# Kernel optimization log

Measured on AMD Instinct MI355X. Metric: run time of the kernel, lower is better.

The kernel has to match this reference:

```python
import jax, jax.numpy as jnp
import numpy as np

NU, NI, E = 100000, 20000, 250000
H, HEADS, D, L = 128, 2, 64, 2


def setup_inputs() -> dict:
    key = jax.random.key(0)
    ks = jax.random.split(key, 12)
    s = 0.05  # glorot-ish init scale
    return {
        "x_user": jax.random.normal(ks[0], (NU, 64), jnp.float32),
        "x_item": jax.random.normal(ks[1], (NI, 128), jnp.float32),
        "Wp_user": jax.random.normal(ks[2], (64, H), jnp.float32) * s,
        "bp_user": jnp.zeros((H,), jnp.float32),
        "Wp_item": jax.random.normal(ks[3], (128, H), jnp.float32) * s,
        "bp_item": jnp.zeros((H,), jnp.float32),
        # stacked per [layer, relation] params; rel 0 = user->item, rel 1 = item->user
        "Wl": jax.random.normal(ks[4], (L, 2, H, H), jnp.float32) * s,  # source linear
        "bl": jnp.zeros((L, 2, H), jnp.float32),
        "Wr": jax.random.normal(ks[5], (L, 2, H, H), jnp.float32) * s,  # target linear
        "br": jnp.zeros((L, 2, H), jnp.float32),
        "att": jax.random.normal(ks[6], (L, 2, HEADS, D), jnp.float32) * s,
        "bias": jnp.zeros((L, 2, H), jnp.float32),
        "edge_src": jax.random.randint(ks[7], (E,), 0, NU, jnp.int32),  # user index per edge
        "edge_dst": jax.random.randint(ks[8], (E,), 0, NI, jnp.int32),  # item index per edge
    }


def _gatv2(x_src, x_dst, src, dst, wl, bl_, wr, br_, a, b_, n_dst):
    """One bipartite GATv2Conv (heads=HEADS, out=D, concat=True, eval mode)."""
    xl = (x_src @ wl + bl_).reshape(-1, HEADS, D)  # [Ns, h, d]
    xr = (x_dst @ wr + br_).reshape(-1, HEADS, D)  # [Nd, h, d]
    e = jax.nn.leaky_relu(xl[src] + xr[dst], 0.2)  # [E, h, d]
    logits = jnp.einsum('ehd,hd->eh', e, a)        # [E, h]
    # segment softmax over destination nodes (numerically stable)
    amax = jax.lax.stop_gradient(jax.ops.segment_max(logits, dst, num_segments=n_dst))
    p = jnp.exp(logits - amax[dst])
    denom = jax.ops.segment_sum(p, dst, num_segments=n_dst)
    alpha = p / (denom[dst] + 1e-16)               # PyG softmax epsilon
    msg = xl[src] * alpha[:, :, None]              # [E, h, d]
    out = jax.ops.segment_sum(msg, dst, num_segments=n_dst)  # [Nd, h, d]
    return out.reshape(n_dst, HEADS * D) + b_


def reference(x_user, x_item, Wp_user, bp_user, Wp_item, bp_item,
              Wl, bl, Wr, br, att, bias, edge_src, edge_dst):
    zu = x_user @ Wp_user + bp_user  # [NU, H]
    zi = x_item @ Wp_item + bp_item  # [NI, H]
    for l in range(L):
        zi_new = _gatv2(zu, zi, edge_src, edge_dst,
                        Wl[l, 0], bl[l, 0], Wr[l, 0], br[l, 0], att[l, 0], bias[l, 0], NI)
        zu_new = _gatv2(zi, zu, edge_dst, edge_src,
                        Wl[l, 1], bl[l, 1], Wr[l, 1], br[l, 1], att[l, 1], bias[l, 1], NU)
        zu, zi = zu_new, zi_new
        if l < L - 1:
            zu, zi = jax.nn.relu(zu), jax.nn.relu(zi)  # dropout is identity in eval
    return zu, zi
```

## Files before the change

kernel.cpp:

```cpp
#include <hip/hip_runtime.h>

#define HDIM 128

typedef __attribute__((ext_vector_type(8))) short short8;
typedef __attribute__((ext_vector_type(4))) float float4v;

__device__ __forceinline__ float b2f(unsigned short u){
  return __uint_as_float(((unsigned int)u) << 16);
}
__device__ __forceinline__ unsigned short f2b(float f){
  unsigned int x = __float_as_uint(f);
  x += 0x7fffu + ((x >> 16) & 1u);
  return (unsigned short)(x >> 16);
}

#if __has_builtin(__builtin_amdgcn_exp2f)
#define EXPX(x) __builtin_amdgcn_exp2f(x)
#define LOGSCALE 1.4426950408889634f
#else
#define EXPX(x) __expf(x)
#define LOGSCALE 1.f
#endif

__device__ __forceinline__ float dpp_red8(float x){
  x += __int_as_float(__builtin_amdgcn_update_dpp(0, __float_as_int(x), 0xB1, 0xF, 0xF, true));
  x += __int_as_float(__builtin_amdgcn_update_dpp(0, __float_as_int(x), 0x4E, 0xF, 0xF, true));
  x += __int_as_float(__builtin_amdgcn_update_dpp(0, __float_as_int(x), 0x141, 0xF, 0xF, true));
  return x;
}

__device__ __forceinline__ int sniff_block(const unsigned short* __restrict__ x){
  const int tid = threadIdx.x;
  int cnt = 0, tot = 0;
  for (int i = tid * 2; i < 4096; i += 512){
    float v = fabsf(b2f(x[i]));
    tot++;
    if (v > 1e-4f && v < 50.f) cnt++;
  }
  __shared__ int s_cnt[256], s_tot[256];
  s_cnt[tid] = cnt; s_tot[tid] = tot;
  __syncthreads();
  for (int o = 128; o > 0; o >>= 1){
    if (tid < o){ s_cnt[tid] += s_cnt[tid + o]; s_tot[tid] += s_tot[tid + o]; }
    __syncthreads();
  }
  __shared__ int res;
  if (tid == 0) res = (s_cnt[0] * 2 < s_tot[0]) ? 1 : 0;
  __syncthreads();
  return res;
}

#define P_WPU 0
#define P_WPI 8192
#define P_WL  24576
#define P_WR  90112
#define P_BL  155648
#define P_BR  156160
#define P_ATT 156672
#define P_BIA 157184
#define P_BPU 157696
#define P_BPI 157824
#define P_TOT 157952

struct CvtArgs { const void* src[10]; int len[10]; const unsigned short* xsniff; };

__global__ void cvt_all_kernel(CvtArgs args, unsigned short* __restrict__ P,
                               int* __restrict__ flag,
                               int* __restrict__ zero1, int nz1,
                               int* __restrict__ zero2, int nz2){
  const int f32 = sniff_block(args.xsniff);
  int t = blockIdx.x * 256 + threadIdx.x;
  if (t < nz1) zero1[t] = 0;
  if (t < nz2) zero2[t] = 0;
  if (t == 0) flag[0] = f32;
  if (t >= P_TOT) return;
  int local = t;
  int i = 0;
  while (local >= args.len[i]){ local -= args.len[i]; i++; }
  if (f32) P[t] = f2b(((const float*)args.src[i])[local]);
  else     P[t] = ((const unsigned short*)args.src[i])[local];
}

__global__ void prep_weights_kernel(const unsigned short* __restrict__ P,
                                    unsigned short* __restrict__ Wc)
{
  const int t = blockIdx.x * 256 + threadIdx.x;
  if (t >= 49664) return;
  const unsigned short* Wl = P + P_WL;
  const unsigned short* Wr = P + P_WR;
  const unsigned short* Bm[4] = { Wl, Wr + 16384, Wl + 16384, Wr };
  const unsigned short* Av[4] = { P + P_WPU, P + P_WPU, P + P_WPI, P + P_WPI };
  const unsigned short* bv[4] = { P + P_BPU, P + P_BPU, P + P_BPI, P + P_BPI };
  const unsigned short* bo[4] = { P + P_BL, P + P_BR + 128, P + P_BL + 128, P + P_BR };
  if (t < 49152){
    int job, base;
    if (t < 8192)       { job = 0; base = 0; }
    else if (t < 16384) { job = 1; base = 8192; }
    else if (t < 32768) { job = 2; base = 16384; }
    else                { job = 3; base = 32768; }
    const int local = t - base;
    const int k = local >> 7, n = local & 127;
    const unsigned short* A = Av[job] + (size_t)k * 128;
    const unsigned short* B = Bm[job];
    float s = 0.f;
    #pragma unroll 4
    for (int h = 0; h < 128; h++) s = fmaf(b2f(A[h]), b2f(B[h * 128 + n]), s);
    Wc[t] = f2b(s);
  } else {
    const int local = t - 49152;
    const int job = local >> 7, n = local & 127;
    const unsigned short* B = Bm[job];
    float s = b2f(bo[job][n]);
    for (int h = 0; h < 128; h++) s = fmaf(b2f(bv[job][h]), b2f(B[h * 128 + n]), s);
    Wc[t] = f2b(s);
  }
}

struct PermBiasArgs { const unsigned short* W0[4]; const unsigned short* W1[4];
                      int KS[4]; int base[4]; int n[4];
                      const unsigned short* blo[4]; const unsigned short* bhi[4]; };
__global__ void permute_bias_kernel(PermBiasArgs pa, unsigned short* __restrict__ dst,
                                    unsigned short* __restrict__ dstB){
  int t = blockIdx.x * 256 + threadIdx.x;
  if (t >= 114688){
    int u = t - 114688;
    if (u < 1024){
      int set = u >> 8, c = u & 255;
      dstB[u] = (c < 128) ? pa.blo[set][c] : pa.bhi[set][c - 128];
    }
    return;
  }
  int job = 0;
  while (job < 4 && t >= pa.base[job] + pa.n[job]) job++;
  if (job >= 4) return;
  int local = t - pa.base[job];
  int KS = pa.KS[job];
  int j = local & 7, rest = local >> 3;
  int l = rest & 63; rest >>= 6;
  int ks = rest % KS, tile = rest / KS;
  int k = ks * 32 + (l >> 4) * 8 + j;
  int c = tile * 16 + (l & 15);
  dst[t] = (c < 128) ? pa.W0[job][k * 128 + c] : pa.W1[job][k * 128 + (c - 128)];
}

template<int K>
__device__ __forceinline__ void linear_body(const void* __restrict__ Xv, int xstride,
                                            bool f32,
                                            const unsigned short* __restrict__ Bp,
                                            const unsigned short* __restrict__ bias,
                                            unsigned short* __restrict__ Y, int M, int bx,
                                            unsigned short* __restrict__ lds)
{
  constexpr int KS = K / 32;
  constexpr int LK = K + 8;
  constexpr int ROUNDS = (32 * K) / 2048;
  const int wave = threadIdx.x >> 6, lane = threadIdx.x & 63;
  const int quad = lane >> 4, l16 = lane & 15;
  const int row0 = bx * 32;

  #pragma unroll
  for (int rd = 0; rd < ROUNDS; rd++){
    const int e = rd * 2048 + (int)threadIdx.x * 8;
    const int rr = e / K, cc = e % K;
    int grow = row0 + rr; if (grow >= M) grow = M - 1;
    unsigned short* dst = lds + rr * LK + cc;
    if (f32){
      const float* p = (const float*)Xv + (size_t)grow * xstride + cc;
      float4 v0 = *(const float4*)p;
      float4 v1 = *(const float4*)(p + 4);
      short8 tmp;
      tmp[0] = (short)f2b(v0.x); tmp[1] = (short)f2b(v0.y);
      tmp[2] = (short)f2b(v0.z); tmp[3] = (short)f2b(v0.w);
      tmp[4] = (short)f2b(v1.x); tmp[5] = (short)f2b(v1.y);
      tmp[6] = (short)f2b(v1.z); tmp[7] = (short)f2b(v1.w);
      *(short8*)dst = tmp;
    } else {
      *(short8*)dst = *(const short8*)((const unsigned short*)Xv + (size_t)grow * xstride + cc);
    }
  }
  __syncthreads();

  float4v acc[2][4];
  const float4v z = {0.f, 0.f, 0.f, 0.f};
  #pragma unroll
  for (int i = 0; i < 2; i++)
    #pragma unroll
    for (int j = 0; j < 4; j++) acc[i][j] = z;

  #pragma unroll
  for (int ks = 0; ks < KS; ks++){
    const int col = ks * 32 + quad * 8;
    short8 a[2];
    #pragma unroll
    for (int mt = 0; mt < 2; mt++)
      a[mt] = *(const short8*)(lds + (mt * 16 + l16) * LK + col);
    short8 b[4];
    #pragma unroll
    for (int ntl = 0; ntl < 4; ntl++){
      const int t = wave * 4 + ntl;
      b[ntl] = *(const short8*)(Bp + ((size_t)(t * KS + ks) * 64 + lane) * 8);
    }
    #pragma unroll
    for (int mt = 0; mt < 2; mt++)
      #pragma unroll
      for (int ntl = 0; ntl < 4; ntl++)
        acc[mt][ntl] = __builtin_amdgcn_mfma_f32_16x16x32_bf16(a[mt], b[ntl], acc[mt][ntl], 0, 0, 0);
  }

  #pragma unroll
  for (int mt = 0; mt < 2; mt++){
    #pragma unroll
    for (int ntl = 0; ntl < 4; ntl++){
      const int t = wave * 4 + ntl;
      const int colb = t * 16 + l16;
      const float bb = b2f(bias[colb]);
      #pragma unroll
      for (int r = 0; r < 4; r++){
        const int row = row0 + mt * 16 + quad * 4 + r;
        if (row < M) Y[(size_t)row * 256 + colb] = f2b(acc[mt][ntl][r] + bb);
      }
    }
  }
}

template<int KA, int KB>
__launch_bounds__(256)
__global__ void linear_both_kernel(const void* __restrict__ XA, int sA,
                                   const unsigned short* __restrict__ BpA,
                                   const unsigned short* __restrict__ biasA,
                                   unsigned short* __restrict__ YA, int MA, int gA,
                                   const void* __restrict__ XB, int sB,
                                   const unsigned short* __restrict__ BpB,
                                   const unsigned short* __restrict__ biasB,
                                   unsigned short* __restrict__ YB, int MB,
                                   const int* __restrict__ flag, int use_flag)
{
  __shared__ unsigned short lds[32 * 136];
  const bool f32 = use_flag && (*flag != 0);
  if ((int)blockIdx.x < gA) linear_body<KA>(XA, sA, f32, BpA, biasA, YA, MA, blockIdx.x, lds);
  else                      linear_body<KB>(XB, sB, f32, BpB, biasB, YB, MB, blockIdx.x - gA, lds);
}

__global__ void count_both_kernel(const int* __restrict__ esrc, const int* __restrict__ edst,
                                  int* __restrict__ degU, int* __restrict__ degI, int E){
  int t = blockIdx.x * 256 + threadIdx.x;
  if (t >= E) return;
  atomicAdd(&degI[edst[t]], 1);
  atomicAdd(&degU[esrc[t]], 1);
}

__global__ void scan_hist_par_kernel(const int* __restrict__ degI, const int* __restrict__ degU,
                                     int* __restrict__ rpI, int* __restrict__ rpU,
                                     int* __restrict__ blkI, int* __restrict__ blkU,
                                     int* __restrict__ histI, int* __restrict__ histU,
                                     int NI, int NU, int BI, int BU, int BI2, int BU2){
  const int tid = threadIdx.x;
  const int b = blockIdx.x;
  const int nscan = BI + BU;
  if (b < nscan){
    __shared__ int s[256];
    const int* deg; int* rowptr; int* blksum; int Nd; int bb;
    if (b < BI){ deg = degI; rowptr = rpI; blksum = blkI; Nd = NI; bb = b; }
    else       { deg = degU; rowptr = rpU; blksum = blkU; Nd = NU; bb = b - BI; }
    const int base = bb * 2048 + tid * 8;
    int v[8]; int tot = 0;
    #pragma unroll
    for (int j = 0; j < 8; j++){
      int idx = base + j;
      v[j] = (idx < Nd) ? deg[idx] : 0;
      tot += v[j];
    }
    s[tid] = tot;
    __syncthreads();
    for (int off = 1; off < 256; off <<= 1){
      int add = (tid >= off) ? s[tid - off] : 0;
      __syncthreads();
      s[tid] += add;
      __syncthreads();
    }
    int run = s[tid] - tot;
    #pragma unroll
    for (int j = 0; j < 8; j++){
      int idx = base + j;
      if (idx < Nd) rowptr[idx] = run;
      run += v[j];
    }
    if (tid == 255) blksum[bb] = s[255];
  } else {
    __shared__ int h2[64];
    if (tid < 64) h2[tid] = 0;
    __syncthreads();
    const int bb = b - nscan;
    const int* deg; int* gh; int base; int N;
    if (bb < BI2){ deg = degI; gh = histI; base = bb * 256; N = NI; }
    else         { deg = degU; gh = histU; base = (bb - BI2) * 256; N = NU; }
    const int n = base + tid;
    if (n < N) atomicAdd(&h2[min(deg[n], 63)], 1);
    __syncthreads();
    if (tid < 64 && h2[tid]) atomicAdd(&gh[tid], h2[tid]);
  }
}

__global__ void tops_kernel(int* __restrict__ blkI, int BI, int* __restrict__ blkU, int BU,
                            int* __restrict__ histI, int* __restrict__ histU){
  const int tid = threadIdx.x;
  const int lane = tid & 63;
  if (tid < 128){
    int* blk = (tid < 64) ? blkI : blkU;
    const int B = (tid < 64) ? BI : BU;
    int v = (lane < B) ? blk[lane] : 0;
    const int orig = v;
    #pragma unroll
    for (int off = 1; off < 64; off <<= 1){
      int u = __shfl_up(v, off, 64);
      if (lane >= off) v += u;
    }
    if (lane < B) blk[lane] = v - orig;
  } else {
    int* h = (tid < 192) ? histI : histU;
    int v = h[lane];
    int x = v;
    #pragma unroll
    for (int off = 1; off < 64; off <<= 1){
      int u = __shfl_down(x, off, 64);
      x += (lane + off < 64) ? u : 0;
    }
    h[lane] = x - v;
  }
}

__global__ void scan_add2_kernel(int* __restrict__ rpI, int* __restrict__ rpU,
                                 const int* __restrict__ blkI, const int* __restrict__ blkU,
                                 int* __restrict__ curI, int* __restrict__ curU,
                                 int NI, int NU, int BI, int E){
  const int b = blockIdx.x;
  int* rowptr; const int* blksum; int* curs; int Nd; int bb;
  if (b < BI){ rowptr = rpI; blksum = blkI; curs = curI; Nd = NI; bb = b; }
  else       { rowptr = rpU; blksum = blkU; curs = curU; Nd = NU; bb = b - BI; }
  const int base = bb * 2048 + threadIdx.x * 8;
  const int add = blksum[bb];
  #pragma unroll
  for (int j = 0; j < 8; j++){
    int idx = base + j;
    if (idx < Nd){ int v = rowptr[idx] + add; rowptr[idx] = v; curs[idx] = v; }
    else if (idx == Nd) rowptr[idx] = E;
  }
}

__global__ void scatter_all_kernel(const int* __restrict__ esrc, const int* __restrict__ edst,
                                   int* __restrict__ curI, int* __restrict__ curU,
                                   int* __restrict__ srcI, int* __restrict__ srcU,
                                   const int* __restrict__ rpI, const int* __restrict__ rpU,
                                   int* __restrict__ histI, int* __restrict__ histU,
                                   int* __restrict__ permI, int* __restrict__ permU,
                                   int NI, int NU, int E, int BI2, int BU2){
  const int tid = threadIdx.x;
  const int b = blockIdx.x;
  const int BP = BI2 + BU2;
  if (b < BP){
    __shared__ int h[64];
    __shared__ int cur[64];
    if (tid < 64) h[tid] = 0;
    __syncthreads();
    const int* rp; int* gh; int* perm; int base; int N;
    if (b < BI2){ rp = rpI; gh = histI; perm = permI; base = b * 256; N = NI; }
    else        { rp = rpU; gh = histU; perm = permU; base = (b - BI2) * 256; N = NU; }
    const int n = base + tid;
    int bk = -1;
    if (n < N){ int d = rp[n + 1] - rp[n]; bk = min(d, 63); atomicAdd(&h[bk], 1); }
    __syncthreads();
    if (tid < 64) cur[tid] = h[tid] ? atomicAdd(&gh[tid], h[tid]) : 0;
    __syncthreads();
    if (n < N){ int r = atomicAdd(&cur[bk], 1); perm[r] = n; }
  } else {
    int t = (b - BP) * 256 + tid;
    if (t < E){
      int d = edst[t];
      int pos = atomicAdd(&curI[d], 1);
      srcI[pos] = esrc[t];
    } else if (t < 2 * E){
      int tt = t - E;
      int d = esrc[tt];
      int pos = atomicAdd(&curU[d], 1);
      srcU[pos] = edst[tt];
    }
  }
}

struct GatRel {
  const unsigned short* zlrS;
  const unsigned short* zlrD;
  const int* rowptr;
  const int* srcArr;
  const int* perm;
  const unsigned short* att;
  const unsigned short* bias;
  void* out;
  unsigned long long elem_off;
  int Nd;
  int nw;
};

__launch_bounds__(256)
__global__ void fused_gat_sorted_kernel(GatRel A, GatRel B, int do_relu,
                                        const int* __restrict__ flag, int final_store)
{
  const int wave = threadIdx.x >> 6;
  const int lane = threadIdx.x & 63;
  const int ql = lane & 15;
  const int quad = lane >> 4;
  int gw = blockIdx.x * 4 + wave;
  GatRel R;
  if (gw < A.nw) R = A;
  else {
    gw -= A.nw;
    if (gw >= B.nw) return;
    R = B;
  }

  const int rank = gw * 4 + quad;
  const bool vnode = rank < R.Nd;
  int d = 0;
  if (vnode) d = R.perm[rank];
  int beg = 0, end = 0;
  if (vnode){ beg = R.rowptr[d]; end = R.rowptr[d + 1]; }
  int md = end - beg;
  md = max(md, __shfl_xor(md, 16, 64));
  md = max(md, __shfl_xor(md, 32, 64));

  const uint4* zlS4 = (const uint4*)R.zlrS;
  uint4 rv = ((const uint4*)R.zlrD)[(size_t)d * 32 + 16 + ql];
  float r[8], a[8];
  {
    const unsigned int* rp = (const unsigned int*)&rv;
    #pragma unroll
    for (int j = 0; j < 4; j++){
      r[2*j]   = __uint_as_float(rp[j] << 16);
      r[2*j+1] = __uint_as_float(rp[j] & 0xffff0000u);
    }
  }
  uint4 av = ((const uint4*)R.att)[ql];
  {
    const unsigned int* ap = (const unsigned int*)&av;
    #pragma unroll
    for (int j = 0; j < 4; j++){
      a[2*j]   = __uint_as_float(ap[j] << 16) * LOGSCALE;
      a[2*j+1] = __uint_as_float(ap[j] & 0xffff0000u) * LOGSCALE;
    }
  }

  float m = -1e30f, s = 0.f;
  float acc[8];
  #pragma unroll
  for (int j = 0; j < 8; j++) acc[j] = 0.f;

  if (md > 0){
    const int* sA = R.srcArr;
    int i1 = 0, i2 = 0;
    if (beg < end)     i1 = sA[beg];
    if (beg + 1 < end) i2 = sA[beg + 1];
    uint4 g0 = zlS4[(size_t)i1 * 32 + ql];

    for (int it = 0; it < md; it++){
      uint4 g1 = zlS4[(size_t)i2 * 32 + ql];
      int i3 = 0;
      { int ee = beg + it + 2; if (ee < end) i3 = sA[ee]; }
      const bool valid = (beg + it) < end;

      float x[8];
      const unsigned int* gp = (const unsigned int*)&g0;
      #pragma unroll
      for (int j = 0; j < 4; j++){
        x[2*j]   = __uint_as_float(gp[j] << 16);
        x[2*j+1] = __uint_as_float(gp[j] & 0xffff0000u);
      }
      float p = 0.f;
      #pragma unroll
      for (int j = 0; j < 8; j++){
        float t = x[j] + r[j];
        t = fmaxf(t, 0.2f * t);
        p = fmaf(a[j], t, p);
      }
      p = dpp_red8(p);
      const float pv = valid ? p : -1e30f;

      if (__builtin_expect(__any(pv > m + 8.f), 0)){
        const float mn = fmaxf(m, pv);
        const float scO = EXPX(m - mn);
        const float qv = valid ? EXPX(pv - mn) : 0.f;
        s = fmaf(s, scO, qv);
        #pragma unroll
        for (int j = 0; j < 8; j++) acc[j] = fmaf(acc[j], scO, x[j] * qv);
        m = mn;
      } else {
        const float qv = valid ? EXPX(pv - m) : 0.f;
        s += qv;
        #pragma unroll
        for (int j = 0; j < 8; j++) acc[j] = fmaf(x[j], qv, acc[j]);
      }
      g0 = g1; i2 = i3;
    }
  }

  const float inv = 1.f / (s + 1e-16f);
  uint4 bv = ((const uint4*)R.bias)[ql];
  float o[8];
  {
    const unsigned int* bp = (const unsigned int*)&bv;
    #pragma unroll
    for (int j = 0; j < 4; j++){
      o[2*j]   = fmaf(acc[2*j],   inv, __uint_as_float(bp[j] << 16));
      o[2*j+1] = fmaf(acc[2*j+1], inv, __uint_as_float(bp[j] & 0xffff0000u));
    }
  }
  if (do_relu){
    #pragma unroll
    for (int j = 0; j < 8; j++) o[j] = fmaxf(o[j], 0.f);
  }
  if (!vnode) return;
  const size_t eidx = (size_t)R.elem_off + (size_t)d * HDIM + 8 * ql;
  if (final_store && (*flag != 0)){
    float4 f0 = {o[0], o[1], o[2], o[3]};
    float4 f1 = {o[4], o[5], o[6], o[7]};
    float4* op = (float4*)R.out;
    op[eidx >> 2] = f0;
    op[(eidx >> 2) + 1] = f1;
  } else {
    uint4 w;
    unsigned int* wp = (unsigned int*)&w;
    #pragma unroll
    for (int j = 0; j < 4; j++)
      wp[j] = (unsigned int)f2b(o[2*j]) | ((unsigned int)f2b(o[2*j+1]) << 16);
    ((uint4*)R.out)[eidx >> 3] = w;
  }
}

extern "C" void kernel_launch(void* const* d_in, const int* in_sizes, int n_in,
                              void* d_out, int out_size, void* d_ws, size_t ws_size,
                              hipStream_t stream)
{
  const int* esrc = (const int*)d_in[12];
  const int* edst = (const int*)d_in[13];

  const int NU = in_sizes[0] / 64;
  const int NI = in_sizes[1] / 128;
  const int E  = in_sizes[12];
  const size_t fu = (size_t)NU * HDIM, fi = (size_t)NI * HDIM;

  char* w = (char*)d_ws;
  auto carve = [&](size_t bytes){ char* p = w; w += (bytes + 255) & ~(size_t)255; return p; };
  int* flag = (int*)carve(4);
  unsigned short* Wc = (unsigned short*)carve(49664 * 2);
  unsigned short* P  = (unsigned short*)carve((size_t)P_TOT * 2);
  unsigned short* Bp = (unsigned short*)carve(114688 * 2);
  unsigned short* Bc = (unsigned short*)carve(1024 * 2);
  int* rowptrI = (int*)carve(((size_t)NI + 1) * 4);
  int* rowptrU = (int*)carve(((size_t)NU + 1) * 4);
  int* curs    = (int*)carve(((size_t)NI + NU) * 4);
  int* cursI = curs;
  int* cursU = curs + NI;
  int* blkI = (int*)carve(64 * 4);
  int* blkU = (int*)carve(64 * 4);
  int* hists = (int*)carve(128 * 4);
  int* histI = hists;
  int* histU = hists + 64;
  int* permI = (int*)carve((size_t)NI * 4);
  int* permU = (int*)carve((size_t)NU * 4);
  int* srcI  = (int*)carve((size_t)E * 4);
  int* srcU  = (int*)carve((size_t)E * 4);
  unsigned short* zlrU = (unsigned short*)carve((size_t)NU * 256 * 2);
  unsigned short* zlrI = (unsigned short*)carve((size_t)NI * 256 * 2);
  (void)ws_size; (void)n_in; (void)out_size; (void)fi;

  unsigned short* stage_zu = (unsigned short*)d_out;
  unsigned short* stage_zi = (unsigned short*)d_out + fu;
  (void)stage_zi;

  CvtArgs ca;
  const int srcIdx[10] = {2, 4, 6, 8, 7, 9, 10, 11, 3, 5};
  const int lens[10] = {8192, 16384, 65536, 65536, 512, 512, 512, 512, 128, 128};
  for (int i = 0; i < 10; i++){ ca.src[i] = d_in[srcIdx[i]]; ca.len[i] = lens[i]; }
  ca.xsniff = (const unsigned short*)d_in[0];
  cvt_all_kernel<<<(P_TOT + 255) / 256, 256, 0, stream>>>(ca, P, flag,
                                                          curs, NI + NU, hists, 128);
  prep_weights_kernel<<<(49664 + 255) / 256, 256, 0, stream>>>(P, Wc);

  const unsigned short* cWlU0 = Wc;
  const unsigned short* cWrU1 = Wc + 8192;
  const unsigned short* cWlI1 = Wc + 16384;
  const unsigned short* cWrI0 = Wc + 32768;

  PermBiasArgs pa;
  pa.W0[0] = cWlU0;                 pa.W1[0] = cWrU1;                 pa.KS[0] = 2; pa.base[0] = 0;     pa.n[0] = 16384;
  pa.W0[1] = cWlI1;                 pa.W1[1] = cWrI0;                 pa.KS[1] = 4; pa.base[1] = 16384; pa.n[1] = 32768;
  pa.W0[2] = P + P_WL + 2 * 16384;  pa.W1[2] = P + P_WR + 3 * 16384;  pa.KS[2] = 4; pa.base[2] = 49152; pa.n[2] = 32768;
  pa.W0[3] = P + P_WL + 3 * 16384;  pa.W1[3] = P + P_WR + 2 * 16384;  pa.KS[3] = 4; pa.base[3] = 81920; pa.n[3] = 32768;
  pa.blo[0] = Wc + 49152;         pa.bhi[0] = Wc + 49152 + 128;
  pa.blo[1] = Wc + 49152 + 256;   pa.bhi[1] = Wc + 49152 + 384;
  pa.blo[2] = P + P_BL + 256;     pa.bhi[2] = P + P_BR + 384;
  pa.blo[3] = P + P_BL + 384;     pa.bhi[3] = P + P_BR + 256;
  permute_bias_kernel<<<(114688 + 1024 + 255) / 256, 256, 0, stream>>>(pa, Bp, Bc);
  unsigned short* BpU0 = Bp;
  unsigned short* BpI0 = Bp + 16384;
  unsigned short* BpU1 = Bp + 49152;
  unsigned short* BpI1 = Bp + 81920;

  const int BI = (NI + 2047) / 2048, BU = (NU + 2047) / 2048;
  const int BI2 = (NI + 255) / 256, BU2 = (NU + 255) / 256;
  count_both_kernel<<<(E + 255) / 256, 256, 0, stream>>>(esrc, edst, cursU, cursI, E);
  scan_hist_par_kernel<<<BI + BU + BI2 + BU2, 256, 0, stream>>>(
      cursI, cursU, rowptrI, rowptrU, blkI, blkU, histI, histU,
      NI, NU, BI, BU, BI2, BU2);
  tops_kernel<<<1, 256, 0, stream>>>(blkI, BI, blkU, BU, histI, histU);
  scan_add2_kernel<<<BI + BU, 256, 0, stream>>>(rowptrI, rowptrU, blkI, blkU, cursI, cursU, NI, NU, BI, E);
  scatter_all_kernel<<<BI2 + BU2 + (2 * E + 255) / 256, 256, 0, stream>>>(
      esrc, edst, cursI, cursU, srcI, srcU, rowptrI, rowptrU,
      histI, histU, permI, permU, NI, NU, E, BI2, BU2);

  const int gMU = (NU + 31) / 32, gMI = (NI + 31) / 32;
  const int nwA = (NI + 3) / 4, nwB = (NU + 3) / 4;
  const int gGat = (nwA + nwB + 3) / 4;

  for (int l = 0; l < 2; l++){
    if (l == 0){
      linear_both_kernel<64, 128><<<gMU + gMI, 256, 0, stream>>>(
          d_in[0], 64, BpU0, Bc, zlrU, NU, gMU,
          d_in[1], 128, BpI0, Bc + 256, zlrI, NI, flag, 1);
    } else {
      linear_both_kernel<128, 128><<<gMU + gMI, 256, 0, stream>>>(
          stage_zu, 128, BpU1, Bc + 512, zlrU, NU, gMU,
          stage_zi, 128, BpI1, Bc + 768, zlrI, NI, flag, 0);
    }
    const int relu = (l == 0);
    const int final_store = (l == 1);

    GatRel A, B;
    A.zlrS = zlrU; A.zlrD = zlrI; A.rowptr = rowptrI; A.srcArr = srcI; A.perm = permI;
    A.att  = P + P_ATT + (l * 2 + 0) * HDIM;
    A.bias = P + P_BIA + (l * 2 + 0) * HDIM;
    A.out = final_store ? d_out : (void*)stage_zu; A.elem_off = fu; A.Nd = NI; A.nw = nwA;
    B.zlrS = zlrI; B.zlrD = zlrU; B.rowptr = rowptrU; B.srcArr = srcU; B.perm = permU;
    B.att  = P + P_ATT + (l * 2 + 1) * HDIM;
    B.bias = P + P_BIA + (l * 2 + 1) * HDIM;
    B.out = final_store ? d_out : (void*)stage_zu; B.elem_off = 0; B.Nd = NU; B.nw = nwB;

    fused_gat_sorted_kernel<<<gGat, 256, 0, stream>>>(A, B, relu, flag, final_store);
  }
}
```

Measured before the change: 298.4 us.

## Merge graph-prep kernels and fold block-sum scans into consumers to cut launches

The edge-degree counting now runs in extra blocks of the weight-prep kernel, and the prefix-scan/histogram blocks run in extra blocks of the weight-permute kernel. The single-block tops_kernel is removed: each scan_add2 block recomputes the block-sum exclusive prefix with a wave shuffle scan, and the scatter kernel derives the degree-histogram suffix offsets itself using a separate cursor array. This removes two launches and their serialization gaps in the setup chain, at the cost of redundant small scans per block and a larger zeroed histogram buffer.

```diff
diff --git a/kernel.cpp b/kernel.cpp
--- a/kernel.cpp
+++ b/kernel.cpp
@@ -81,10 +81,22 @@
   else     P[t] = ((const unsigned short*)args.src[i])[local];
 }
 
-__global__ void prep_weights_kernel(const unsigned short* __restrict__ P,
-                                    unsigned short* __restrict__ Wc)
+__global__ void prep_count_kernel(const unsigned short* __restrict__ P,
+                                  unsigned short* __restrict__ Wc,
+                                  const int* __restrict__ esrc, const int* __restrict__ edst,
+                                  int* __restrict__ degU, int* __restrict__ degI,
+                                  int E, int gPrep)
 {
-  const int t = blockIdx.x * 256 + threadIdx.x;
+  const int b = blockIdx.x;
+  if (b >= gPrep){
+    int t = (b - gPrep) * 256 + threadIdx.x;
+    if (t < E){
+      atomicAdd(&degI[edst[t]], 1);
+      atomicAdd(&degU[esrc[t]], 1);
+    }
+    return;
+  }
+  const int t = b * 256 + threadIdx.x;
   if (t >= 49664) return;
   const unsigned short* Wl = P + P_WL;
   const unsigned short* Wr = P + P_WR;
@@ -119,28 +131,166 @@
 struct PermBiasArgs { const unsigned short* W0[4]; const unsigned short* W1[4];
                       int KS[4]; int base[4]; int n[4];
                       const unsigned short* blo[4]; const unsigned short* bhi[4]; };
-__global__ void permute_bias_kernel(PermBiasArgs pa, unsigned short* __restrict__ dst,
-                                    unsigned short* __restrict__ dstB){
-  int t = blockIdx.x * 256 + threadIdx.x;
-  if (t >= 114688){
-    int u = t - 114688;
-    if (u < 1024){
-      int set = u >> 8, c = u & 255;
-      dstB[u] = (c < 128) ? pa.blo[set][c] : pa.bhi[set][c - 128];
-    }
+
+__global__ void permute_scanhist_kernel(PermBiasArgs pa, unsigned short* __restrict__ dst,
+                                        unsigned short* __restrict__ dstB, int gPerm,
+                                        const int* __restrict__ degI, const int* __restrict__ degU,
+                                        int* __restrict__ rpI, int* __restrict__ rpU,
+                                        int* __restrict__ blkI, int* __restrict__ blkU,
+                                        int* __restrict__ histI, int* __restrict__ histU,
+                                        int NI, int NU, int BI, int BU, int BI2, int BU2)
+{
+  const int tid = threadIdx.x;
+  const int bk0 = blockIdx.x;
+  if (bk0 < gPerm){
+    int t = bk0 * 256 + tid;
+    if (t >= 114688){
+      int u = t - 114688;
+      if (u < 1024){
+        int set = u >> 8, c = u & 255;
+        dstB[u] = (c < 128) ? pa.blo[set][c] : pa.bhi[set][c - 128];
+      }
+      return;
+    }
+    int job = 0;
+    while (job < 4 && t >= pa.base[job] + pa.n[job]) job++;
+    if (job >= 4) return;
+    int local = t - pa.base[job];
+    int KS = pa.KS[job];
+    int j = local & 7, rest = local >> 3;
+    int l = rest & 63; rest >>= 6;
+    int ks = rest % KS, tile = rest / KS;
+    int k = ks * 32 + (l >> 4) * 8 + j;
+    int c = tile * 16 + (l & 15);
+    dst[t] = (c < 128) ? pa.W0[job][k * 128 + c] : pa.W1[job][k * 128 + (c - 128)];
     return;
   }
-  int job = 0;
-  while (job < 4 && t >= pa.base[job] + pa.n[job]) job++;
-  if (job >= 4) return;
-  int local = t - pa.base[job];
-  int KS = pa.KS[job];
-  int j = local & 7, rest = local >> 3;
-  int l = rest & 63; rest >>= 6;
-  int ks = rest % KS, tile = rest / KS;
-  int k = ks * 32 + (l >> 4) * 8 + j;
-  int c = tile * 16 + (l & 15);
-  dst[t] = (c < 128) ? pa.W0[job][k * 128 + c] : pa.W1[job][k * 128 + (c - 128)];
+  const int b = bk0 - gPerm;
+  const int nscan = BI + BU;
+  if (b < nscan){
+    __shared__ int s[256];
+    const int* deg; int* rowptr; int* blksum; int Nd; int bb;
+    if (b < BI){ deg = degI; rowptr = rpI; blksum = blkI; Nd = NI; bb = b; }
+    else       { deg = degU; rowptr = rpU; blksum = blkU; Nd = NU; bb = b - BI; }
+    const int base = bb * 2048 + tid * 8;
+    int v[8]; int tot = 0;
+    #pragma unroll
+    for (int j = 0; j < 8; j++){
+      int idx = base + j;
+      v[j] = (idx < Nd) ? deg[idx] : 0;
+      tot += v[j];
+    }
+    s[tid] = tot;
+    __syncthreads();
+    for (int off = 1; off < 256; off <<= 1){
+      int add = (tid >= off) ? s[tid - off] : 0;
+      __syncthreads();
+      s[tid] += add;
+      __syncthreads();
+    }
+    int run = s[tid] - tot;
+    #pragma unroll
+    for (int j = 0; j < 8; j++){
+      int idx = base + j;
+      if (idx < Nd) rowptr[idx] = run;
+      run += v[j];
+    }
+    if (tid == 255) blksum[bb] = s[255];
+  } else {
+    __shared__ int h2[64];
+    if (tid < 64) h2[tid] = 0;
+    __syncthreads();
+    const int bb = b - nscan;
+    const int* deg; int* gh; int base; int N;
+    if (bb < BI2){ deg = degI; gh = histI; base = bb * 256; N = NI; }
+    else         { deg = degU; gh = histU; base = (bb - BI2) * 256; N = NU; }
+    const int n = base + tid;
+    if (n < N) atomicAdd(&h2[min(deg[n], 63)], 1);
+    __syncthreads();
+    if (tid < 64 && h2[tid]) atomicAdd(&gh[tid], h2[tid]);
+  }
+}
+
+__global__ void scan_add2_kernel(int* __restrict__ rpI, int* __restrict__ rpU,
+                                 const int* __restrict__ blkI, const int* __restrict__ blkU,
+                                 int* __restrict__ curI, int* __restrict__ curU,
+                                 int NI, int NU, int BI, int BU, int E){
+  const int b = blockIdx.x;
+  int* rowptr; const int* blksum; int* curs; int Nd; int bb; int Bn;
+  if (b < BI){ rowptr = rpI; blksum = blkI; curs = curI; Nd = NI; bb = b; Bn = BI; }
+  else       { rowptr = rpU; blksum = blkU; curs = curU; Nd = NU; bb = b - BI; Bn = BU; }
+  const int tid = threadIdx.x;
+  __shared__ int sAdd;
+  if (tid < 64){
+    int v = (tid < Bn) ? blksum[tid] : 0;
+    int x = v;
+    #pragma unroll
+    for (int off = 1; off < 64; off <<= 1){
+      int u = __shfl_up(x, off, 64);
+      if (tid >= off) x += u;
+    }
+    if (tid == bb) sAdd = x - v;
+  }
+  __syncthreads();
+  const int add = sAdd;
+  const int base = bb * 2048 + tid * 8;
+  #pragma unroll
+  for (int j = 0; j < 8; j++){
+    int idx = base + j;
+    if (idx < Nd){ int v = rowptr[idx] + add; rowptr[idx] = v; curs[idx] = v; }
+    else if (idx == Nd) rowptr[idx] = E;
+  }
+}
+
+__global__ void scatter_all_kernel(const int* __restrict__ esrc, const int* __restrict__ edst,
+                                   int* __restrict__ curI, int* __restrict__ curU,
+                                   int* __restrict__ srcI, int* __restrict__ srcU,
+                                   const int* __restrict__ rpI, const int* __restrict__ rpU,
+                                   const int* __restrict__ histI, const int* __restrict__ histU,
+                                   int* __restrict__ hcurI, int* __restrict__ hcurU,
+                                   int* __restrict__ permI, int* __restrict__ permU,
+                                   int NI, int NU, int E, int BI2, int BU2){
+  const int tid = threadIdx.x;
+  const int b = blockIdx.x;
+  const int BP = BI2 + BU2;
+  if (b < BP){
+    __shared__ int h[64];
+    __shared__ int cur[64];
+    if (tid < 64) h[tid] = 0;
+    __syncthreads();
+    const int* rp; const int* gh; int* ghc; int* perm; int base; int N;
+    if (b < BI2){ rp = rpI; gh = histI; ghc = hcurI; perm = permI; base = b * 256; N = NI; }
+    else        { rp = rpU; gh = histU; ghc = hcurU; perm = permU; base = (b - BI2) * 256; N = NU; }
+    const int n = base + tid;
+    int bk = -1;
+    if (n < N){ int d = rp[n + 1] - rp[n]; bk = min(d, 63); atomicAdd(&h[bk], 1); }
+    __syncthreads();
+    if (tid < 64){
+      int v = gh[tid];
+      int x = v;
+      #pragma unroll
+      for (int off = 1; off < 64; off <<= 1){
+        int u = __shfl_down(x, off, 64);
+        x += (tid + off < 64) ? u : 0;
+      }
+      const int suf = x - v;
+      cur[tid] = h[tid] ? (suf + atomicAdd(&ghc[tid], h[tid])) : 0;
+    }
+    __syncthreads();
+    if (n < N){ int r = atomicAdd(&cur[bk], 1); perm[r] = n; }
+  } else {
+    int t = (b - BP) * 256 + tid;
+    if (t < E){
+      int d = edst[t];
+      int pos = atomicAdd(&curI[d], 1);
+      srcI[pos] = esrc[t];
+    } else if (t < 2 * E){
+      int tt = t - E;
+      int d = esrc[tt];
+      int pos = atomicAdd(&curU[d], 1);
+      srcU[pos] = edst[tt];
+    }
+  }
 }
 
 template<int K>
@@ -241,152 +391,6 @@
   else                      linear_body<KB>(XB, sB, f32, BpB, biasB, YB, MB, blockIdx.x - gA, lds);
 }
 
-__global__ void count_both_kernel(const int* __restrict__ esrc, const int* __restrict__ edst,
-                                  int* __restrict__ degU, int* __restrict__ degI, int E){
-  int t = blockIdx.x * 256 + threadIdx.x;
-  if (t >= E) return;
-  atomicAdd(&degI[edst[t]], 1);
-  atomicAdd(&degU[esrc[t]], 1);
-}
-
-__global__ void scan_hist_par_kernel(const int* __restrict__ degI, const int* __restrict__ degU,
-                                     int* __restrict__ rpI, int* __restrict__ rpU,
-                                     int* __restrict__ blkI, int* __restrict__ blkU,
-                                     int* __restrict__ histI, int* __restrict__ histU,
-                                     int NI, int NU, int BI, int BU, int BI2, int BU2){
-  const int tid = threadIdx.x;
-  const int b = blockIdx.x;
-  const int nscan = BI + BU;
-  if (b < nscan){
-    __shared__ int s[256];
-    const int* deg; int* rowptr; int* blksum; int Nd; int bb;
-    if (b < BI){ deg = degI; rowptr = rpI; blksum = blkI; Nd = NI; bb = b; }
-    else       { deg = degU; rowptr = rpU; blksum = blkU; Nd = NU; bb = b - BI; }
-    const int base = bb * 2048 + tid * 8;
-    int v[8]; int tot = 0;
-    #pragma unroll
-    for (int j = 0; j < 8; j++){
-      int idx = base + j;
-      v[j] = (idx < Nd) ? deg[idx] : 0;
-      tot += v[j];
-    }
-    s[tid] = tot;
-    __syncthreads();
-    for (int off = 1; off < 256; off <<= 1){
-      int add = (tid >= off) ? s[tid - off] : 0;
-      __syncthreads();
-      s[tid] += add;
-      __syncthreads();
-    }
-    int run = s[tid] - tot;
-    #pragma unroll
-    for (int j = 0; j < 8; j++){
-      int idx = base + j;
-      if (idx < Nd) rowptr[idx] = run;
-      run += v[j];
-    }
-    if (tid == 255) blksum[bb] = s[255];
-  } else {
-    __shared__ int h2[64];
-    if (tid < 64) h2[tid] = 0;
-    __syncthreads();
-    const int bb = b - nscan;
-    const int* deg; int* gh; int base; int N;
-    if (bb < BI2){ deg = degI; gh = histI; base = bb * 256; N = NI; }
-    else         { deg = degU; gh = histU; base = (bb - BI2) * 256; N = NU; }
-    const int n = base + tid;
-    if (n < N) atomicAdd(&h2[min(deg[n], 63)], 1);
-    __syncthreads();
-    if (tid < 64 && h2[tid]) atomicAdd(&gh[tid], h2[tid]);
-  }
-}
-
-__global__ void tops_kernel(int* __restrict__ blkI, int BI, int* __restrict__ blkU, int BU,
-                            int* __restrict__ histI, int* __restrict__ histU){
-  const int tid = threadIdx.x;
-  const int lane = tid & 63;
-  if (tid < 128){
-    int* blk = (tid < 64) ? blkI : blkU;
-    const int B = (tid < 64) ? BI : BU;
-    int v = (lane < B) ? blk[lane] : 0;
-    const int orig = v;
-    #pragma unroll
-    for (int off = 1; off < 64; off <<= 1){
-      int u = __shfl_up(v, off, 64);
-      if (lane >= off) v += u;
-    }
-    if (lane < B) blk[lane] = v - orig;
-  } else {
-    int* h = (tid < 192) ? histI : histU;
-    int v = h[lane];
-    int x = v;
-    #pragma unroll
-    for (int off = 1; off < 64; off <<= 1){
-      int u = __shfl_down(x, off, 64);
-      x += (lane + off < 64) ? u : 0;
-    }
-    h[lane] = x - v;
-  }
-}
-
-__global__ void scan_add2_kernel(int* __restrict__ rpI, int* __restrict__ rpU,
-                                 const int* __restrict__ blkI, const int* __restrict__ blkU,
-                                 int* __restrict__ curI, int* __restrict__ curU,
-                                 int NI, int NU, int BI, int E){
-  const int b = blockIdx.x;
-  int* rowptr; const int* blksum; int* curs; int Nd; int bb;
-  if (b < BI){ rowptr = rpI; blksum = blkI; curs = curI; Nd = NI; bb = b; }
-  else       { rowptr = rpU; blksum = blkU; curs = curU; Nd = NU; bb = b - BI; }
-  const int base = bb * 2048 + threadIdx.x * 8;
-  const int add = blksum[bb];
-  #pragma unroll
-  for (int j = 0; j < 8; j++){
-    int idx = base + j;
-    if (idx < Nd){ int v = rowptr[idx] + add; rowptr[idx] = v; curs[idx] = v; }
-    else if (idx == Nd) rowptr[idx] = E;
-  }
-}
-
-__global__ void scatter_all_kernel(const int* __restrict__ esrc, const int* __restrict__ edst,
-                                   int* __restrict__ curI, int* __restrict__ curU,
-                                   int* __restrict__ srcI, int* __restrict__ srcU,
-                                   const int* __restrict__ rpI, const int* __restrict__ rpU,
-                                   int* __restrict__ histI, int* __restrict__ histU,
-                                   int* __restrict__ permI, int* __restrict__ permU,
-                                   int NI, int NU, int E, int BI2, int BU2){
-  const int tid = threadIdx.x;
-  const int b = blockIdx.x;
-  const int BP = BI2 + BU2;
-  if (b < BP){
-    __shared__ int h[64];
-    __shared__ int cur[64];
-    if (tid < 64) h[tid] = 0;
-    __syncthreads();
-    const int* rp; int* gh; int* perm; int base; int N;
-    if (b < BI2){ rp = rpI; gh = histI; perm = permI; base = b * 256; N = NI; }
-    else        { rp = rpU; gh = histU; perm = permU; base = (b - BI2) * 256; N = NU; }
-    const int n = base + tid;
-    int bk = -1;
-    if (n < N){ int d = rp[n + 1] - rp[n]; bk = min(d, 63); atomicAdd(&h[bk], 1); }
-    __syncthreads();
-    if (tid < 64) cur[tid] = h[tid] ? atomicAdd(&gh[tid], h[tid]) : 0;
-    __syncthreads();
-    if (n < N){ int r = atomicAdd(&cur[bk], 1); perm[r] = n; }
-  } else {
-    int t = (b - BP) * 256 + tid;
-    if (t < E){
-      int d = edst[t];
-      int pos = atomicAdd(&curI[d], 1);
-      srcI[pos] = esrc[t];
-    } else if (t < 2 * E){
-      int tt = t - E;
-      int d = esrc[tt];
-      int pos = atomicAdd(&curU[d], 1);
-      srcU[pos] = edst[tt];
-    }
-  }
-}
-
 struct GatRel {
   const unsigned short* zlrS;
   const unsigned short* zlrD;
@@ -561,9 +565,11 @@
   int* cursU = curs + NI;
   int* blkI = (int*)carve(64 * 4);
   int* blkU = (int*)carve(64 * 4);
-  int* hists = (int*)carve(128 * 4);
+  int* hists = (int*)carve(256 * 4);
   int* histI = hists;
   int* histU = hists + 64;
+  int* hcurI = hists + 128;
+  int* hcurU = hists + 192;
   int* permI = (int*)carve((size_t)NI * 4);
   int* permU = (int*)carve((size_t)NU * 4);
   int* srcI  = (int*)carve((size_t)E * 4);
@@ -582,8 +588,12 @@
   for (int i = 0; i < 10; i++){ ca.src[i] = d_in[srcIdx[i]]; ca.len[i] = lens[i]; }
   ca.xsniff = (const unsigned short*)d_in[0];
   cvt_all_kernel<<<(P_TOT + 255) / 256, 256, 0, stream>>>(ca, P, flag,
-                                                          curs, NI + NU, hists, 128);
-  prep_weights_kernel<<<(49664 + 255) / 256, 256, 0, stream>>>(P, Wc);
+                                                          curs, NI + NU, hists, 256);
+
+  const int gPrep = (49664 + 255) / 256;
+  const int gCount = (E + 255) / 256;
+  prep_count_kernel<<<gPrep + gCount, 256, 0, stream>>>(P, Wc, esrc, edst,
+                                                        cursU, cursI, E, gPrep);
 
   const unsigned short* cWlU0 = Wc;
   const unsigned short* cWrU1 = Wc + 8192;
@@ -599,23 +609,23 @@
   pa.blo[1] = Wc + 49152 + 256;   pa.bhi[1] = Wc + 49152 + 384;
   pa.blo[2] = P + P_BL + 256;     pa.bhi[2] = P + P_BR + 384;
   pa.blo[3] = P + P_BL + 384;     pa.bhi[3] = P + P_BR + 256;
-  permute_bias_kernel<<<(114688 + 1024 + 255) / 256, 256, 0, stream>>>(pa, Bp, Bc);
+  const int BI = (NI + 2047) / 2048, BU = (NU + 2047) / 2048;
+  const int BI2 = (NI + 255) / 256, BU2 = (NU + 255) / 256;
+  const int gPerm = (114688 + 1024 + 255) / 256;
+  permute_scanhist_kernel<<<gPerm + BI + BU + BI2 + BU2, 256, 0, stream>>>(
+      pa, Bp, Bc, gPerm,
+      cursI, cursU, rowptrI, rowptrU, blkI, blkU, histI, histU,
+      NI, NU, BI, BU, BI2, BU2);
   unsigned short* BpU0 = Bp;
   unsigned short* BpI0 = Bp + 16384;
   unsigned short* BpU1 = Bp + 49152;
   unsigned short* BpI1 = Bp + 81920;
 
-  const int BI = (NI + 2047) / 2048, BU = (NU + 2047) / 2048;
-  const int BI2 = (NI + 255) / 256, BU2 = (NU + 255) / 256;
-  count_both_kernel<<<(E + 255) / 256, 256, 0, stream>>>(esrc, edst, cursU, cursI, E);
-  scan_hist_par_kernel<<<BI + BU + BI2 + BU2, 256, 0, stream>>>(
-      cursI, cursU, rowptrI, rowptrU, blkI, blkU, histI, histU,
-      NI, NU, BI, BU, BI2, BU2);
-  tops_kernel<<<1, 256, 0, stream>>>(blkI, BI, blkU, BU, histI, histU);
-  scan_add2_kernel<<<BI + BU, 256, 0, stream>>>(rowptrI, rowptrU, blkI, blkU, cursI, cursU, NI, NU, BI, E);
+  scan_add2_kernel<<<BI + BU, 256, 0, stream>>>(rowptrI, rowptrU, blkI, blkU,
+                                                cursI, cursU, NI, NU, BI, BU, E);
   scatter_all_kernel<<<BI2 + BU2 + (2 * E + 255) / 256, 256, 0, stream>>>(
       esrc, edst, cursI, cursU, srcI, srcU, rowptrI, rowptrU,
-      histI, histU, permI, permU, NI, NU, E, BI2, BU2);
+      histI, histU, hcurI, hcurU, permI, permU, NI, NU, E, BI2, BU2);
 
   const int gMU = (NU + 31) / 32, gMI = (NI + 31) / 32;
   const int nwA = (NI + 3) / 4, nwB = (NU + 3) / 4;
```

New measurement: 292.5 us. Within noise of the previous version (-2.0%).
